# Optimization experiments

Hardware: AMD Instinct MI355X
Metric: run time of the kernel (lower is better)

Reference implementation:

```python
import jax, jax.numpy as jnp
import numpy as np

B, N, D = 8, 1024, 256
H = 8
DH = D // H
R = 4          # relation types 0..3; adj value 4 = no relation
FF = 1024
EPS = 1e-5


def _lin(k, fan_in, shape):
    return jax.random.normal(k, shape, jnp.float32) * (1.0 / np.sqrt(fan_in))


def setup_inputs() -> dict:
    key = jax.random.key(0)
    ks = jax.random.split(key, 16)
    src = jax.random.normal(ks[0], (B, N, D), jnp.float32)
    adj_matrix = jax.random.randint(ks[1], (B, N, N), 0, 5, dtype=jnp.int32)
    Wq = _lin(ks[2], D, (D, D)); bq = jnp.zeros((D,), jnp.float32)
    Wk = _lin(ks[3], D, (D, D)); bk = jnp.zeros((D,), jnp.float32)
    Wv = _lin(ks[4], D, (R, D, D)); bv = jnp.zeros((R, D), jnp.float32)
    Wo = _lin(ks[5], D, (D, D)); bo = jnp.zeros((D,), jnp.float32)
    W1 = _lin(ks[6], D, (D, FF)); b1 = jnp.zeros((FF,), jnp.float32)
    W2 = _lin(ks[7], FF, (FF, D)); b2 = jnp.zeros((D,), jnp.float32)
    g1 = jnp.ones((D,), jnp.float32); beta1 = jnp.zeros((D,), jnp.float32)
    g2 = jnp.ones((D,), jnp.float32); beta2 = jnp.zeros((D,), jnp.float32)
    return dict(src=src, adj_matrix=adj_matrix, Wq=Wq, bq=bq, Wk=Wk, bk=bk,
                Wv=Wv, bv=bv, Wo=Wo, bo=bo, W1=W1, b1=b1, W2=W2, b2=b2,
                g1=g1, beta1=beta1, g2=g2, beta2=beta2)


def _ln(x, g, b):
    m = x.mean(-1, keepdims=True)
    v = ((x - m) ** 2).mean(-1, keepdims=True)
    return (x - m) * jax.lax.rsqrt(v + EPS) * g + b


def reference(src, adj_matrix, Wq, bq, Wk, bk, Wv, bv, Wo, bo, W1, b1, W2, b2, g1, beta1, g2, beta2):
    Bb, Nn, Dm = src.shape
    h, dh = H, Dm // H
    q = (src @ Wq + bq).reshape(Bb, Nn, h, dh).transpose(0, 2, 1, 3)  # (B,H,N,dh)
    k = (src @ Wk + bk).reshape(Bb, Nn, h, dh).transpose(0, 2, 1, 3)
    scores = jnp.einsum('bhid,bhjd->bhij', q, k) / np.sqrt(dh)
    attn = jax.nn.softmax(scores, axis=-1)                             # (B,H,N,N)
    out = jnp.zeros_like(q)
    for r in range(Wv.shape[0]):  # small fixed relation loop, matches module
        v_r = (src @ Wv[r] + bv[r]).reshape(Bb, Nn, h, dh).transpose(0, 2, 1, 3)
        mask = (adj_matrix == r)[:, None]                              # (B,1,N,N)
        out = out + jnp.einsum('bhij,bhjd->bhid', attn * mask, v_r)
    attn_out = out.transpose(0, 2, 1, 3).reshape(Bb, Nn, Dm) @ Wo + bo
    x = _ln(src + attn_out, g1, beta1)
    ff = jax.nn.gelu(x @ W1 + b1, approximate=False) @ W2 + b2
    return _ln(x + ff, g2, beta2)
```

## Files before the change

kernel.cpp:

```cpp
#include <hip/hip_runtime.h>
#include <hip/hip_bf16.h>
#include <cmath>

constexpr int CB  = 8;
constexpr int CN  = 1024;
constexpr int CD  = 256;
constexpr int CH  = 8;
constexpr int CDH = 32;
constexpr int CR  = 4;
constexpr int CFF = 1024;
constexpr float CEPS = 1e-5f;
constexpr size_t SZH = (size_t)CB * CH * CN * CDH;

#define MODE_QK    0
#define MODE_FFN1  2
#define MODE_VT    4

typedef float v4f __attribute__((ext_vector_type(4)));
typedef short v8s __attribute__((ext_vector_type(8)));

static __device__ __forceinline__ short f2bf(float f) {
    unsigned u = __builtin_bit_cast(unsigned, f);
    u += 0x7fff + ((u >> 16) & 1);
    return (short)(u >> 16);
}

static __device__ __forceinline__ void async_copy16(const void* g, void* l) {
    __builtin_amdgcn_global_load_lds(
        (const __attribute__((address_space(1))) void*)g,
        (__attribute__((address_space(3))) void*)l, 16, 0, 0);
}

template<int BM, int BN, int MODE>
__device__ __forceinline__ void gemm_body(
    const short* __restrict__ A, const short* __restrict__ Bw,
    const float* __restrict__ biasv, void* __restrict__ dest,
    int M, int K, int Nw, int bx, int by, short* smem)
{
    constexpr int WTM = BM / 2, WTN = BN / 2;
    constexpr int TM = WTM / 16, TN = WTN / 16;
    short* As = smem;
    short* Bs = smem + 2 * BM * 32;

    const int t    = threadIdx.x;
    const int lane = t & 63;
    const int w    = t >> 6;
    const int quad = lane >> 4, l15 = lane & 15;
    const int wm = w >> 1, wn = w & 1;
    const int m0 = bx * BM, n0 = by * BN;

    const int srow = lane >> 2;
    const int scol = (lane & 3) * 8;

    v4f acc[TM][TN];
    #pragma unroll
    for (int i = 0; i < TM; ++i)
        #pragma unroll
        for (int j = 0; j < TN; ++j) acc[i][j] = (v4f){0.f, 0.f, 0.f, 0.f};

    const int NK = K >> 5;

    auto stage = [&](int buf, int kt) {
        #pragma unroll
        for (int u = 0; u < BM / 64; ++u) {
            const int e0 = (w * (BM / 64) + u) * 512;
            const int row = (e0 >> 5) + srow;
            async_copy16(A + (size_t)(m0 + row) * K + kt + scol,
                         &As[buf * BM * 32 + e0]);
        }
        #pragma unroll
        for (int u = 0; u < BN / 64; ++u) {
            const int e0 = (w * (BN / 64) + u) * 512;
            const int row = (e0 >> 5) + srow;
            async_copy16(Bw + (size_t)(n0 + row) * K + kt + scol,
                         &Bs[buf * BN * 32 + e0]);
        }
    };

    stage(0, 0);

    for (int it = 0; it < NK; ++it) {
        __syncthreads();
        if (it + 1 < NK) stage((it + 1) & 1, (it + 1) << 5);

        const int buf = it & 1;
        v8s af[TM], bfr[TN];
        #pragma unroll
        for (int i = 0; i < TM; ++i)
            af[i] = *(const v8s*)&As[buf * BM * 32 +
                                     (wm * WTM + i * 16 + l15) * 32 + quad * 8];
        #pragma unroll
        for (int j = 0; j < TN; ++j)
            bfr[j] = *(const v8s*)&Bs[buf * BN * 32 +
                                      (wn * WTN + j * 16 + l15) * 32 + quad * 8];
        #pragma unroll
        for (int i = 0; i < TM; ++i)
            #pragma unroll
            for (int j = 0; j < TN; ++j)
                acc[i][j] = __builtin_amdgcn_mfma_f32_16x16x32_bf16(
                    af[i], bfr[j], acc[i][j], 0, 0, 0);
    }

    #pragma unroll
    for (int i = 0; i < TM; ++i) {
        #pragma unroll
        for (int j = 0; j < TN; ++j) {
            const int mb = m0 + wm * WTM + i * 16 + quad * 4;
            const int n  = n0 + wn * WTN + j * 16 + l15;
            float vals[4];
            if (MODE == MODE_VT) {
                #pragma unroll
                for (int rr = 0; rr < 4; ++rr) vals[rr] = acc[i][j][rr] + biasv[mb + rr];
            } else {
                #pragma unroll
                for (int rr = 0; rr < 4; ++rr) vals[rr] = acc[i][j][rr] + biasv[n];
            }

            if (MODE == MODE_QK) {
                const int b = mb >> 10, ii0 = mb & 1023;
                const int plane = n >> 8, nn = n & 255;
                const int h = nn >> 5, d = nn & 31;
                #pragma unroll
                for (int rr = 0; rr < 4; ++rr)
                    ((short*)dest)[(size_t)plane * SZH +
                        (((size_t)(b * CH + h)) * CN + ii0 + rr) * CDH + d] =
                        f2bf(vals[rr]);
            } else if (MODE == MODE_VT) {
                const int b = n >> 10, ii = n & 1023;
                #pragma unroll
                for (int rr = 0; rr < 4; ++rr) {
                    const int m = mb + rr;
                    const int r2 = m >> 8, hd = m & 255;
                    const int h = hd >> 5, d = hd & 31;
                    ((short*)dest)[2 * SZH +
                        (((size_t)(r2 * 64 + b * CH + h)) * CDH + d) * CN + ii] =
                        f2bf(vals[rr]);
                }
            } else {
                #pragma unroll
                for (int rr = 0; rr < 4; ++rr) {
                    const size_t idx = (size_t)(mb + rr) * Nw + n;
                    const float xx = vals[rr];
                    const float E = exp2f(2.302217f * (xx + 0.044715f * xx * xx * xx));
                    ((short*)dest)[idx] = f2bf(xx * E / (E + 1.f));
                }
            }
        }
    }
}

template<int BM, int BN, int MODE>
__global__ __launch_bounds__(256)
void gemm_mfma(const short* __restrict__ A, const short* __restrict__ Bw,
               const float* __restrict__ biasv, void* __restrict__ dest,
               int M, int K, int Nw)
{
    extern __shared__ short smem[];
    gemm_body<BM, BN, MODE>(A, Bw, biasv, dest, M, K, Nw,
                            blockIdx.x, blockIdx.y, smem);
}

__global__ __launch_bounds__(256)
void proj_kernel(const short* __restrict__ src_bf, const short* __restrict__ wqkvT,
                 const float* __restrict__ bpack, short* __restrict__ qkv)
{
    extern __shared__ short smem[];
    const int g = blockIdx.x;
    if (g < 512) {
        gemm_body<64, 128, MODE_QK>(src_bf, wqkvT, bpack, qkv,
                                    8192, 256, 512, g >> 2, g & 3, smem);
    } else {
        const int h2 = g - 512;
        gemm_body<64, 128, MODE_VT>(wqkvT + 512 * 256, src_bf, bpack + 512,
                                    qkv, 1024, 256, 8192, h2 & 15, h2 >> 4, smem);
    }
}

template<bool WRITE_BF>
__global__ __launch_bounds__(256)
void gemm_ln(const short* __restrict__ A, const short* __restrict__ Bw,
             const float* __restrict__ biasv, const float* __restrict__ add,
             const float* __restrict__ gw, const float* __restrict__ be,
             float* __restrict__ outf, short* __restrict__ outb, int K)
{
    __shared__ short As[2][64 * 32];
    __shared__ short Bs[2][256 * 32];

    const int t    = threadIdx.x;
    const int lane = t & 63;
    const int w    = t >> 6;
    const int quad = lane >> 4, l15 = lane & 15;
    const int m0   = blockIdx.x * 64;

    const int srow = lane >> 2;
    const int scol = (lane & 3) * 8;

    v4f acc[16];
    #pragma unroll
    for (int j = 0; j < 16; ++j) acc[j] = (v4f){0.f, 0.f, 0.f, 0.f};

    const int NK = K >> 5;

    auto stage = [&](int buf, int kt) {
        async_copy16(A + (size_t)(m0 + 16 * w + srow) * K + kt + scol,
                     &As[buf][w * 512]);
        #pragma unroll
        for (int u = 0; u < 4; ++u) {
            const int e0 = (w * 4 + u) * 512;
            async_copy16(Bw + (size_t)((e0 >> 5) + srow) * K + kt + scol,
                         &Bs[buf][e0]);
        }
    };

    stage(0, 0);

    for (int it = 0; it < NK; ++it) {
        __syncthreads();
        if (it + 1 < NK) stage((it + 1) & 1, (it + 1) << 5);

        const int buf = it & 1;
        const v8s af = *(const v8s*)&As[buf][(16 * w + l15) * 32 + quad * 8];
        #pragma unroll
        for (int j = 0; j < 16; ++j) {
            const v8s bfr = *(const v8s*)&Bs[buf][(16 * j + l15) * 32 + quad * 8];
            acc[j] = __builtin_amdgcn_mfma_f32_16x16x32_bf16(af, bfr, acc[j], 0, 0, 0);
        }
    }

    #pragma unroll
    for (int rr = 0; rr < 4; ++rr) {
        const int row = m0 + 16 * w + quad * 4 + rr;
        float v[16];
        float s = 0.f;
        #pragma unroll
        for (int j = 0; j < 16; ++j) {
            const int n = 16 * j + l15;
            v[j] = acc[j][rr] + biasv[n] + add[(size_t)row * CD + n];
            s += v[j];
        }
        #pragma unroll
        for (int off = 1; off < 16; off <<= 1) s += __shfl_xor(s, off);
        const float mean = s * (1.f / CD);
        float s2 = 0.f;
        #pragma unroll
        for (int j = 0; j < 16; ++j) { v[j] -= mean; s2 += v[j] * v[j]; }
        #pragma unroll
        for (int off = 1; off < 16; off <<= 1) s2 += __shfl_xor(s2, off);
        const float rstd = rsqrtf(s2 * (1.f / CD) + CEPS);
        #pragma unroll
        for (int j = 0; j < 16; ++j) {
            const int n = 16 * j + l15;
            const float y = v[j] * rstd * gw[n] + be[n];
            outf[(size_t)row * CD + n] = y;
            if (WRITE_BF) outb[(size_t)row * CD + n] = f2bf(y);
        }
    }
}

__global__ __launch_bounds__(256)
void prep(const int* __restrict__ adj, const float* __restrict__ src,
          const float* __restrict__ Wq, const float* __restrict__ Wk,
          const float* __restrict__ Wv, const float* __restrict__ Wo,
          const float* __restrict__ W1, const float* __restrict__ W2,
          const float* __restrict__ bq, const float* __restrict__ bk,
          const float* __restrict__ bv, const float* __restrict__ bo,
          const float* __restrict__ b1, const float* __restrict__ b2,
          unsigned char* __restrict__ adj8, short* __restrict__ src_bf,
          short* __restrict__ wqkvT, short* __restrict__ woT,
          short* __restrict__ w1T, short* __restrict__ w2T,
          float* __restrict__ bpack)
{
    __shared__ float tile[64][65];
    const int bx = blockIdx.x, t = threadIdx.x;
    if (bx < 8192) {
        const int i = bx * 256 + t;
        const int4 vv = ((const int4*)adj)[i];
        uchar4 c;
        c.x = (unsigned char)vv.x; c.y = (unsigned char)vv.y;
        c.z = (unsigned char)vv.z; c.w = (unsigned char)vv.w;
        ((uchar4*)adj8)[i] = c;
    } else if (bx < 10240) {
        const int i = (bx - 8192) * 256 + t;
        const float4 v = ((const float4*)src)[i];
        short4 o;
        o.x = f2bf(v.x); o.y = f2bf(v.y); o.z = f2bf(v.z); o.w = f2bf(v.w);
        ((short4*)src_bf)[i] = o;
    } else if (bx < 10480) {
        const int tt = bx - 10240;
        const float* S; short* D;
        int Sstride, Dstride, k0, srccol, dstrow;
        if (tt < 96) {
            const int tk = tt & 3, tn = tt >> 2;
            const int ng = tn * 64;
            Sstride = 256; Dstride = 256; k0 = tk * 64;
            dstrow = tn * 64; D = wqkvT;
            if (ng < 256)      { S = Wq; srccol = ng; }
            else if (ng < 512) { S = Wk; srccol = ng - 256; }
            else { const int r = (ng - 512) >> 8;
                   S = Wv + (size_t)r * 65536; srccol = (ng - 512) & 255; }
        } else if (tt < 112) {
            const int u = tt - 96, tk = u & 3, tn = u >> 2;
            S = Wo; Sstride = 256; D = woT; Dstride = 256;
            k0 = tk * 64; srccol = tn * 64; dstrow = tn * 64;
        } else if (tt < 176) {
            const int u = tt - 112, tk = u & 3, tn = u >> 2;
            S = W1; Sstride = 1024; D = w1T; Dstride = 256;
            k0 = tk * 64; srccol = tn * 64; dstrow = tn * 64;
        } else {
            const int u = tt - 176, tk = u & 15, tn = u >> 4;
            S = W2; Sstride = 256; D = w2T; Dstride = 1024;
            k0 = tk * 64; srccol = tn * 64; dstrow = tn * 64;
        }
        #pragma unroll
        for (int u2 = 0; u2 < 4; ++u2) {
            const int kl = (t >> 4) + u2 * 16;
            const int nl = (t & 15) * 4;
            const float4 v = *(const float4*)&S[(size_t)(k0 + kl) * Sstride + srccol + nl];
            tile[kl][nl + 0] = v.x; tile[kl][nl + 1] = v.y;
            tile[kl][nl + 2] = v.z; tile[kl][nl + 3] = v.w;
        }
        __syncthreads();
        #pragma unroll
        for (int u2 = 0; u2 < 4; ++u2) {
            const int nl = (t >> 4) + u2 * 16;
            const int kl = (t & 15) * 4;
            short4 o;
            o.x = f2bf(tile[kl + 0][nl]); o.y = f2bf(tile[kl + 1][nl]);
            o.z = f2bf(tile[kl + 2][nl]); o.w = f2bf(tile[kl + 3][nl]);
            *(short4*)&D[(size_t)(dstrow + nl) * Dstride + k0 + kl] = o;
        }
    } else {
        const int idx = (bx - 10480) * 256 + t;
        float bvv;
        if (idx < 256)       bvv = bq[idx];
        else if (idx < 512)  bvv = bk[idx - 256];
        else if (idx < 1536) bvv = bv[idx - 512];
        else if (idx < 1792) bvv = bo[idx - 1536];
        else if (idx < 2816) bvv = b1[idx - 1792];
        else                 bvv = b2[idx - 2816];
        bpack[idx] = bvv;
    }
}

__global__ __launch_bounds__(256)
void attn_mfma(const short* __restrict__ qg, const short* __restrict__ kg,
               const short* __restrict__ vt, const unsigned char* __restrict__ adj8,
               short* __restrict__ outh)
{
    __shared__ __align__(16) short ks[64 * 32];
    __shared__ __align__(16) short vtile[4][32][72];
    __shared__ __align__(16) short ps[64][68];
    __shared__ __align__(16) unsigned char adjs[64][72];
    __shared__ int lut[64][4];

    const int t    = threadIdx.x;
    const int lane = t & 63;
    const int w    = t >> 6;
    const int quad = lane >> 4;
    const int l15  = lane & 15;
    const int i0   = blockIdx.x * 64;
    const int h    = blockIdx.y;
    const int b    = blockIdx.z;
    const int bhh  = b * CH + h;
    const size_t bh = (size_t)bhh;

    if (t < 64) {
        const int b0 = t & 7, b1 = t >> 3;
        #pragma unroll
        for (int r = 0; r < 4; ++r) {
            const int lo = (b0 == r) ? 0x0100 : 0x0c0c;
            const int hi = (b1 == r) ? 0x0302 : 0x0c0c;
            lut[t][r] = lo | (hi << 16);
        }
    }

    const v8s qfrag = *(const v8s*)&qg[(bh * CN + i0 + 16 * w + l15) * CDH + quad * 8];

    v4f oacc[2];
    oacc[0] = (v4f){0.f, 0.f, 0.f, 0.f};
    oacc[1] = (v4f){0.f, 0.f, 0.f, 0.f};
    float plsum[4] = {0.f, 0.f, 0.f, 0.f};

    const float cs = 0.25503480f;
    const int arow = 16 * w + l15;

    const int srow = lane >> 2;
    const int scol = (lane & 3) * 8;
    const int vd0  = lane >> 3;
    const int vc   = (lane & 7) * 8;
    const short* vplane = vt + (((size_t)(w * 64 + bhh)) * CDH) * CN;
    const int aro = t >> 2;
    const int aco = (t & 3) * 16;

    for (int jt = 0; jt < 16; ++jt) {
        const int j0 = jt * 64;
        __syncthreads();

        async_copy16(kg + (bh * CN + j0 + 16 * w + srow) * CDH + scol,
                     &ks[(16 * w + srow) * 32]);
        #pragma unroll
        for (int it = 0; it < 4; ++it) {
            const int d = vd0 + 8 * it;
            const v8s vv = *(const v8s*)&vplane[(size_t)d * CN + j0 + vc];
            *(v8s*)&vtile[w][d][vc] = vv;
        }
        const int4 av = *(const int4*)&adj8[((size_t)b * CN + i0 + aro) * CN + j0 + aco];
        *(int4*)&adjs[aro][aco] = av;
        __syncthreads();

        v4f sacc[4];
        #pragma unroll
        for (int jb = 0; jb < 4; ++jb) {
            const v8s kfrag = *(const v8s*)&ks[(16 * jb + l15) * 32 + quad * 8];
            sacc[jb] = __builtin_amdgcn_mfma_f32_16x16x32_bf16(
                qfrag, kfrag, (v4f){0.f, 0.f, 0.f, 0.f}, 0, 0, 0);
        }

        #pragma unroll
        for (int rr = 0; rr < 4; ++rr) {
            const int prow = 16 * w + quad * 4 + rr;
            float p[4];
            #pragma unroll
            for (int jb = 0; jb < 4; ++jb) p[jb] = exp2f(cs * sacc[jb][rr]);
            plsum[rr] += (p[0] + p[1]) + (p[2] + p[3]);
            #pragma unroll
            for (int jb = 0; jb < 4; ++jb)
                ps[prow][16 * jb + l15] = f2bf(p[jb]);
        }

        #pragma unroll
        for (int kb = 0; kb < 2; ++kb) {
            const int2 p0 = *(const int2*)&ps[arow][32 * kb + quad * 8];
            const int2 p1 = *(const int2*)&ps[arow][32 * kb + quad * 8 + 4];
            const int2 ab = *(const int2*)&adjs[arow][32 * kb + quad * 8];
            int pf[4][4];
            #pragma unroll
            for (int half = 0; half < 2; ++half) {
                const unsigned a = (unsigned)(half ? ab.y : ab.x);
                const int P0 = half ? p1.x : p0.x;
                const int P1 = half ? p1.y : p0.y;
                const int idxA = (a & 7) | ((a >> 5) & 0x38);
                const int idxB = ((a >> 16) & 7) | ((a >> 21) & 0x38);
                const int4 selA = *(const int4*)&lut[idxA][0];
                const int4 selB = *(const int4*)&lut[idxB][0];
                pf[0][half * 2 + 0] = __builtin_amdgcn_perm(P0, P0, selA.x);
                pf[1][half * 2 + 0] = __builtin_amdgcn_perm(P0, P0, selA.y);
                pf[2][half * 2 + 0] = __builtin_amdgcn_perm(P0, P0, selA.z);
                pf[3][half * 2 + 0] = __builtin_amdgcn_perm(P0, P0, selA.w);
                pf[0][half * 2 + 1] = __builtin_amdgcn_perm(P1, P1, selB.x);
                pf[1][half * 2 + 1] = __builtin_amdgcn_perm(P1, P1, selB.y);
                pf[2][half * 2 + 1] = __builtin_amdgcn_perm(P1, P1, selB.z);
                pf[3][half * 2 + 1] = __builtin_amdgcn_perm(P1, P1, selB.w);
            }
            #pragma unroll
            for (int r = 0; r < 4; ++r) {
                const v8s pfr = __builtin_bit_cast(v8s,
                    make_int4(pf[r][0], pf[r][1], pf[r][2], pf[r][3]));
                #pragma unroll
                for (int cb = 0; cb < 2; ++cb) {
                    const v8s vfrag = *(const v8s*)&vtile[r][16 * cb + l15][32 * kb + quad * 8];
                    oacc[cb] = __builtin_amdgcn_mfma_f32_16x16x32_bf16(
                        pfr, vfrag, oacc[cb], 0, 0, 0);
                }
            }
        }
    }

    #pragma unroll
    for (int rr = 0; rr < 4; ++rr) {
        float l = plsum[rr];
        #pragma unroll
        for (int off = 1; off < 16; off <<= 1) l += __shfl_xor(l, off);
        const float inv = 1.f / l;
        const int row = i0 + 16 * w + quad * 4 + rr;
        #pragma unroll
        for (int cb = 0; cb < 2; ++cb)
            outh[((size_t)b * CN + row) * CD + h * CDH + 16 * cb + l15] =
                f2bf(oacc[cb][rr] * inv);
    }
}

extern "C" void kernel_launch(void* const* d_in, const int* in_sizes, int n_in,
                              void* d_out, int out_size, void* d_ws, size_t ws_size,
                              hipStream_t stream)
{
    const float* src = (const float*)d_in[0];
    const int*   adj = (const int*)d_in[1];
    const float* Wq  = (const float*)d_in[2];
    const float* bq  = (const float*)d_in[3];
    const float* Wk  = (const float*)d_in[4];
    const float* bk  = (const float*)d_in[5];
    const float* Wv  = (const float*)d_in[6];
    const float* bv  = (const float*)d_in[7];
    const float* Wo  = (const float*)d_in[8];
    const float* bo  = (const float*)d_in[9];
    const float* W1  = (const float*)d_in[10];
    const float* b1  = (const float*)d_in[11];
    const float* W2  = (const float*)d_in[12];
    const float* b2  = (const float*)d_in[13];
    const float* g1  = (const float*)d_in[14];
    const float* be1 = (const float*)d_in[15];
    const float* g2  = (const float*)d_in[16];
    const float* be2 = (const float*)d_in[17];
    float* out = (float*)d_out;

    char* wsb = (char*)d_ws;
    const size_t MB = (size_t)1 << 20;

    unsigned char* adj8 = (unsigned char*)(wsb);
    short* qkv_bf = (short*)(wsb + 8 * MB);
    short* src_bf = (short*)(wsb + 32 * MB);
    short* wqkvT  = (short*)(wsb + 36 * MB);
    short* woT    = (short*)(wsb + 36 * MB + 768 * 1024);
    short* w1T    = (short*)(wsb + 36 * MB + 896 * 1024);
    short* w2T    = (short*)(wsb + 36 * MB + 1408 * 1024);
    float* bpack  = (float*)(wsb + 36 * MB + 1920 * 1024);
    short* heads_bf = (short*)(wsb + 38 * MB);
    float* xres   = (float*)(wsb + 42 * MB);
    short* x_bf   = (short*)(wsb + 32 * MB);
    short* h1_bf  = (short*)(wsb + 16 * MB);

    const int M = CB * CN;
    dim3 blk(256);

    prep<<<dim3(10492), blk, 0, stream>>>(adj, src, Wq, Wk, Wv, Wo, W1, W2,
        bq, bk, bv, bo, b1, b2, adj8, src_bf, wqkvT, woT, w1T, w2T, bpack);

    proj_kernel<<<dim3(1536), blk, 24576, stream>>>(src_bf, wqkvT, bpack, qkv_bf);

    attn_mfma<<<dim3(CN / 64, CH, CB), blk, 0, stream>>>(
        qkv_bf, qkv_bf + SZH, qkv_bf + 2 * SZH, adj8, heads_bf);

    gemm_ln<true><<<dim3(M / 64), blk, 0, stream>>>(
        heads_bf, woT, bpack + 1536, src, g1, be1, xres, x_bf, CD);

    gemm_mfma<64, 128, MODE_FFN1><<<dim3(M / 64, CFF / 128), blk, 24576, stream>>>(
        x_bf, w1T, bpack + 1792, h1_bf, M, CD, CFF);

    gemm_ln<false><<<dim3(M / 64), blk, 0, stream>>>(
        h1_bf, w2T, bpack + 2816, xres, g2, be2, out, nullptr, CFF);
}
```

Baseline: 255.2 us.

## Halve gemm_ln row tile with cross-wave LN reduction; move adj conversion into proj kernel

The fused GEMM+LayerNorm kernels now use 32-row tiles, with each pair of waves splitting the 256 output columns. Row sums and sums of squares are combined through shared memory, and variance is computed in one pass. This doubles the block count to 256 and fills more of the CUs, at the cost of a barrier and a less numerically stable variance formula. The int32 to uint8 adjacency conversion also moves out of prep into 512 extra grid-stride blocks of the projection kernel. There it overlaps with the QKV GEMMs instead of running as a separate bandwidth-bound phase.

After: 246.1 us. 3.6% less time.

```diff
diff --git a/kernel.cpp b/kernel.cpp
--- a/kernel.cpp
+++ b/kernel.cpp
@@ -162,48 +162,62 @@
 
 __global__ __launch_bounds__(256)
 void proj_kernel(const short* __restrict__ src_bf, const short* __restrict__ wqkvT,
-                 const float* __restrict__ bpack, short* __restrict__ qkv)
+                 const float* __restrict__ bpack, short* __restrict__ qkv,
+                 const int* __restrict__ adj, unsigned char* __restrict__ adj8)
 {
     extern __shared__ short smem[];
     const int g = blockIdx.x;
     if (g < 512) {
         gemm_body<64, 128, MODE_QK>(src_bf, wqkvT, bpack, qkv,
                                     8192, 256, 512, g >> 2, g & 3, smem);
-    } else {
+    } else if (g < 1536) {
         const int h2 = g - 512;
         gemm_body<64, 128, MODE_VT>(wqkvT + 512 * 256, src_bf, bpack + 512,
                                     qkv, 1024, 256, 8192, h2 & 15, h2 >> 4, smem);
+    } else {
+        const int n4 = CB * CN * CN / 4;
+        for (int i = (g - 1536) * 256 + threadIdx.x; i < n4; i += 512 * 256) {
+            const int4 vv = ((const int4*)adj)[i];
+            uchar4 c;
+            c.x = (unsigned char)vv.x; c.y = (unsigned char)vv.y;
+            c.z = (unsigned char)vv.z; c.w = (unsigned char)vv.w;
+            ((uchar4*)adj8)[i] = c;
+        }
     }
 }
 
 template<bool WRITE_BF>
 __global__ __launch_bounds__(256)
-void gemm_ln(const short* __restrict__ A, const short* __restrict__ Bw,
-             const float* __restrict__ biasv, const float* __restrict__ add,
-             const float* __restrict__ gw, const float* __restrict__ be,
-             float* __restrict__ outf, short* __restrict__ outb, int K)
-{
-    __shared__ short As[2][64 * 32];
+void gemm_ln32(const short* __restrict__ A, const short* __restrict__ Bw,
+               const float* __restrict__ biasv, const float* __restrict__ add,
+               const float* __restrict__ gw, const float* __restrict__ be,
+               float* __restrict__ outf, short* __restrict__ outb, int K)
+{
+    __shared__ short As[2][32 * 32];
     __shared__ short Bs[2][256 * 32];
+    __shared__ float redS[2][16][2], redQ[2][16][2];
 
     const int t    = threadIdx.x;
     const int lane = t & 63;
     const int w    = t >> 6;
     const int quad = lane >> 4, l15 = lane & 15;
-    const int m0   = blockIdx.x * 64;
+    const int wr   = w >> 1;
+    const int wg   = w & 1;
+    const int m0   = blockIdx.x * 32;
 
     const int srow = lane >> 2;
     const int scol = (lane & 3) * 8;
 
-    v4f acc[16];
+    v4f acc[8];
     #pragma unroll
-    for (int j = 0; j < 16; ++j) acc[j] = (v4f){0.f, 0.f, 0.f, 0.f};
+    for (int j = 0; j < 8; ++j) acc[j] = (v4f){0.f, 0.f, 0.f, 0.f};
 
     const int NK = K >> 5;
 
     auto stage = [&](int buf, int kt) {
-        async_copy16(A + (size_t)(m0 + 16 * w + srow) * K + kt + scol,
-                     &As[buf][w * 512]);
+        if (w < 2)
+            async_copy16(A + (size_t)(m0 + 16 * w + srow) * K + kt + scol,
+                         &As[buf][w * 512]);
         #pragma unroll
         for (int u = 0; u < 4; ++u) {
             const int e0 = (w * 4 + u) * 512;
@@ -219,38 +233,51 @@
         if (it + 1 < NK) stage((it + 1) & 1, (it + 1) << 5);
 
         const int buf = it & 1;
-        const v8s af = *(const v8s*)&As[buf][(16 * w + l15) * 32 + quad * 8];
-        #pragma unroll
-        for (int j = 0; j < 16; ++j) {
-            const v8s bfr = *(const v8s*)&Bs[buf][(16 * j + l15) * 32 + quad * 8];
+        const v8s af = *(const v8s*)&As[buf][(16 * wr + l15) * 32 + quad * 8];
+        #pragma unroll
+        for (int j = 0; j < 8; ++j) {
+            const v8s bfr = *(const v8s*)&Bs[buf][(wg * 128 + 16 * j + l15) * 32 + quad * 8];
             acc[j] = __builtin_amdgcn_mfma_f32_16x16x32_bf16(af, bfr, acc[j], 0, 0, 0);
         }
     }
 
+    float v[4][8];
     #pragma unroll
     for (int rr = 0; rr < 4; ++rr) {
-        const int row = m0 + 16 * w + quad * 4 + rr;
-        float v[16];
-        float s = 0.f;
-        #pragma unroll
-        for (int j = 0; j < 16; ++j) {
-            const int n = 16 * j + l15;
-            v[j] = acc[j][rr] + biasv[n] + add[(size_t)row * CD + n];
-            s += v[j];
-        }
-        #pragma unroll
-        for (int off = 1; off < 16; off <<= 1) s += __shfl_xor(s, off);
+        const int row = m0 + 16 * wr + quad * 4 + rr;
+        float s = 0.f, sq = 0.f;
+        #pragma unroll
+        for (int j = 0; j < 8; ++j) {
+            const int n = wg * 128 + 16 * j + l15;
+            const float x = acc[j][rr] + biasv[n] + add[(size_t)row * CD + n];
+            v[rr][j] = x;
+            s += x; sq += x * x;
+        }
+        #pragma unroll
+        for (int off = 1; off < 16; off <<= 1) {
+            s  += __shfl_xor(s, off);
+            sq += __shfl_xor(sq, off);
+        }
+        if (l15 == 0) {
+            redS[wr][quad * 4 + rr][wg] = s;
+            redQ[wr][quad * 4 + rr][wg] = sq;
+        }
+    }
+    __syncthreads();
+
+    #pragma unroll
+    for (int rr = 0; rr < 4; ++rr) {
+        const int r16 = quad * 4 + rr;
+        const int row = m0 + 16 * wr + r16;
+        const float s  = redS[wr][r16][0] + redS[wr][r16][1];
+        const float sq = redQ[wr][r16][0] + redQ[wr][r16][1];
         const float mean = s * (1.f / CD);
-        float s2 = 0.f;
-        #pragma unroll
-        for (int j = 0; j < 16; ++j) { v[j] -= mean; s2 += v[j] * v[j]; }
-        #pragma unroll
-        for (int off = 1; off < 16; off <<= 1) s2 += __shfl_xor(s2, off);
-        const float rstd = rsqrtf(s2 * (1.f / CD) + CEPS);
-        #pragma unroll
-        for (int j = 0; j < 16; ++j) {
-            const int n = 16 * j + l15;
-            const float y = v[j] * rstd * gw[n] + be[n];
+        const float var  = sq * (1.f / CD) - mean * mean;
+        const float rstd = rsqrtf(var + CEPS);
+        #pragma unroll
+        for (int j = 0; j < 8; ++j) {
+            const int n = wg * 128 + 16 * j + l15;
+            const float y = (v[rr][j] - mean) * rstd * gw[n] + be[n];
             outf[(size_t)row * CD + n] = y;
             if (WRITE_BF) outb[(size_t)row * CD + n] = f2bf(y);
         }
@@ -258,35 +285,28 @@
 }
 
 __global__ __launch_bounds__(256)
-void prep(const int* __restrict__ adj, const float* __restrict__ src,
+void prep(const float* __restrict__ src,
           const float* __restrict__ Wq, const float* __restrict__ Wk,
           const float* __restrict__ Wv, const float* __restrict__ Wo,
           const float* __restrict__ W1, const float* __restrict__ W2,
           const float* __restrict__ bq, const float* __restrict__ bk,
           const float* __restrict__ bv, const float* __restrict__ bo,
           const float* __restrict__ b1, const float* __restrict__ b2,
-          unsigned char* __restrict__ adj8, short* __restrict__ src_bf,
+          short* __restrict__ src_bf,
           short* __restrict__ wqkvT, short* __restrict__ woT,
           short* __restrict__ w1T, short* __restrict__ w2T,
           float* __restrict__ bpack)
 {
     __shared__ float tile[64][65];
     const int bx = blockIdx.x, t = threadIdx.x;
-    if (bx < 8192) {
+    if (bx < 2048) {
         const int i = bx * 256 + t;
-        const int4 vv = ((const int4*)adj)[i];
-        uchar4 c;
-        c.x = (unsigned char)vv.x; c.y = (unsigned char)vv.y;
-        c.z = (unsigned char)vv.z; c.w = (unsigned char)vv.w;
-        ((uchar4*)adj8)[i] = c;
-    } else if (bx < 10240) {
-        const int i = (bx - 8192) * 256 + t;
         const float4 v = ((const float4*)src)[i];
         short4 o;
         o.x = f2bf(v.x); o.y = f2bf(v.y); o.z = f2bf(v.z); o.w = f2bf(v.w);
         ((short4*)src_bf)[i] = o;
-    } else if (bx < 10480) {
-        const int tt = bx - 10240;
+    } else if (bx < 2288) {
+        const int tt = bx - 2048;
         const float* S; short* D;
         int Sstride, Dstride, k0, srccol, dstrow;
         if (tt < 96) {
@@ -330,7 +350,7 @@
             *(short4*)&D[(size_t)(dstrow + nl) * Dstride + k0 + kl] = o;
         }
     } else {
-        const int idx = (bx - 10480) * 256 + t;
+        const int idx = (bx - 2288) * 256 + t;
         float bvv;
         if (idx < 256)       bvv = bq[idx];
         else if (idx < 512)  bvv = bk[idx - 256];
@@ -523,20 +543,21 @@
     const int M = CB * CN;
     dim3 blk(256);
 
-    prep<<<dim3(10492), blk, 0, stream>>>(adj, src, Wq, Wk, Wv, Wo, W1, W2,
-        bq, bk, bv, bo, b1, b2, adj8, src_bf, wqkvT, woT, w1T, w2T, bpack);
-
-    proj_kernel<<<dim3(1536), blk, 24576, stream>>>(src_bf, wqkvT, bpack, qkv_bf);
+    prep<<<dim3(2300), blk, 0, stream>>>(src, Wq, Wk, Wv, Wo, W1, W2,
+        bq, bk, bv, bo, b1, b2, src_bf, wqkvT, woT, w1T, w2T, bpack);
+
+    proj_kernel<<<dim3(2048), blk, 24576, stream>>>(
+        src_bf, wqkvT, bpack, qkv_bf, adj, adj8);
 
     attn_mfma<<<dim3(CN / 64, CH, CB), blk, 0, stream>>>(
         qkv_bf, qkv_bf + SZH, qkv_bf + 2 * SZH, adj8, heads_bf);
 
-    gemm_ln<true><<<dim3(M / 64), blk, 0, stream>>>(
+    gemm_ln32<true><<<dim3(M / 32), blk, 0, stream>>>(
         heads_bf, woT, bpack + 1536, src, g1, be1, xres, x_bf, CD);
 
     gemm_mfma<64, 128, MODE_FFN1><<<dim3(M / 64, CFF / 128), blk, 24576, stream>>>(
         x_bf, w1T, bpack + 1792, h1_bf, M, CD, CFF);
 
-    gemm_ln<false><<<dim3(M / 64), blk, 0, stream>>>(
+    gemm_ln32<false><<<dim3(M / 32), blk, 0, stream>>>(
         h1_bf, w2T, bpack + 2816, xres, g2, be2, out, nullptr, CFF);
 }
```
